# Performance work log

Hardware: AMD Instinct MI355X
Metric: run time of the kernel (lower is better)

## Reference

```python
import jax, jax.numpy as jnp
import numpy as np

B, L, C_IN = 32, 244, 128
F_NUM, KS = 64, 5
HID = 512
SA_DIV = 3
F3 = F_NUM * 3
D_SA = F3 // SA_DIV  # must equal F_NUM (sa_div==3) for the view in SelfAttention


def setup_inputs() -> dict:
    key = jax.random.key(0)
    ks = jax.random.split(key, 16)

    def rn(k, shape, fan_in):
        return jax.random.normal(k, shape, dtype=jnp.float32) * float(np.sqrt(2.0 / fan_in))

    return {
        "x": jax.random.normal(ks[0], (B, L, C_IN), dtype=jnp.float32),
        "conv1_w": rn(ks[1], (F_NUM, 1, KS, 1), KS),
        "conv1_b": jnp.zeros((F_NUM,), jnp.float32),
        "conv2_w": rn(ks[2], (F_NUM, F_NUM, KS, 1), F_NUM * KS),
        "conv2_b": jnp.zeros((F_NUM,), jnp.float32),
        "conv3_w": rn(ks[3], (F_NUM, F_NUM, KS, 1), F_NUM * KS),
        "conv3_b": jnp.zeros((F_NUM,), jnp.float32),
        "conv4_w": rn(ks[4], (F_NUM, F_NUM, KS, 1), F_NUM * KS),
        "conv4_b": jnp.zeros((F_NUM,), jnp.float32),
        "wq": rn(ks[5], (D_SA, F3), F3),
        "wk": rn(ks[6], (D_SA, F3), F3),
        "wv": rn(ks[7], (D_SA, F3), F3),
        "wv1": rn(ks[8], (D_SA, F3), F3),
        "gamma": jnp.full((1,), 0.1, jnp.float32),
        "gru_wih": rn(ks[9], (3 * HID, F_NUM * C_IN), F_NUM * C_IN),
        "gru_whh": rn(ks[10], (3 * HID, HID), HID),
        "gru_bih": jnp.zeros((3 * HID,), jnp.float32),
        "gru_bhh": jnp.zeros((3 * HID,), jnp.float32),
        "fc_w": rn(ks[11], (1, HID), HID),
        "fc_b": jnp.zeros((1,), jnp.float32),
    }


def _conv2d(x, w, b):
    y = jax.lax.conv_general_dilated(
        x, w, window_strides=(1, 1), padding="VALID",
        dimension_numbers=("NCHW", "OIHW", "NCHW"))
    return y + b[None, :, None, None]


def reference(x, conv1_w, conv1_b, conv2_w, conv2_b, conv3_w, conv3_b, conv4_w, conv4_b,
              wq, wk, wv, wv1, gamma, gru_wih, gru_whh, gru_bih, gru_bhh, fc_w, fc_b):
    # conv stack: (B,1,L,C) -> (B,F,L',C), time dim shrinks by 4*(KS-1)
    h = x[:, None, :, :]
    h = jax.nn.relu(_conv2d(h, conv1_w, conv1_b))
    h = jax.nn.relu(_conv2d(h, conv2_w, conv2_b))
    h = jax.nn.relu(_conv2d(h, conv3_w, conv3_b))
    h = jax.nn.relu(_conv2d(h, conv4_w, conv4_b))
    Bn, Fn, Lp, Cn = h.shape
    step = int(np.ceil(Lp / 3))
    # static slice starts; last slice is x[:, :, -3:, :] (matches torch loop)
    starts = np.minimum(np.arange(step) * 3, Lp - 3)
    idx = starts[:, None] + np.arange(3)                               # (S,3)
    xs = h[:, :, idx, :]                                               # (B,F,S,3,C)
    xs = xs.transpose(0, 2, 1, 3, 4).reshape(Bn, step, Fn * 3, Cn)     # (B,S,F3,C)
    # batched SelfAttention (1x1 conv1d == matmul over channel dim)
    f = jnp.einsum("df,bsfc->bsdc", wq, xs)
    g = jnp.einsum("df,bsfc->bsdc", wk, xs)
    v = jnp.einsum("df,bsfc->bsdc", wv, xs)
    v1 = jnp.einsum("df,bsfc->bsdc", wv1, xs)
    # torch: softmax(bmm(f^T, g), dim=1) -> softmax over first C axis
    beta = jax.nn.softmax(jnp.einsum("bsdc,bsdk->bsck", f, g), axis=-2)
    o = gamma[0] * jnp.einsum("bsdc,bsck->bsdk", v, beta) + v1         # (B,S,F,C)
    seq = o.transpose(1, 0, 2, 3).reshape(step, Bn, Fn * Cn)           # (S,B,F*C)
    # single-layer GRU (PyTorch gate order r,z,n), seq-first
    xg = jnp.einsum("sbi,gi->sbg", seq, gru_wih) + gru_bih             # (S,B,3H)

    def gru_step(hprev, xg_t):
        hg = hprev @ gru_whh.T + gru_bhh
        xr, xz, xn = jnp.split(xg_t, 3, axis=-1)
        hr, hz, hn = jnp.split(hg, 3, axis=-1)
        r = jax.nn.sigmoid(xr + hr)
        z = jax.nn.sigmoid(xz + hz)
        n = jnp.tanh(xn + r * hn)
        hnew = (1.0 - z) * n + z * hprev
        return hnew, hnew

    h0 = jnp.zeros((Bn, HID), seq.dtype)
    _, outs = jax.lax.scan(gru_step, h0, xg)                            # (S,B,H)
    # temporal attention pooling over the time axis (axis 0)
    att = jnp.einsum("sbh,h->sb", outs, fc_w[0]) + fc_b[0]
    w_att = jax.nn.softmax(att, axis=0)[:, :, None]
    return jnp.sum(w_att * outs, axis=0)                                # (B,H)
```

## Files before the change

kernel.cpp:

```cpp
#include <hip/hip_runtime.h>
#include <math.h>


typedef __attribute__((ext_vector_type(8))) short short8;
typedef __attribute__((ext_vector_type(4))) float f32x4;

#define XG_STRIDE 3735552ull

__device__ inline float sigm(float x){ return 1.f/(1.f+__expf(-x)); }
__device__ inline unsigned short f2bf(float f){
    unsigned int u = __float_as_uint(f);
    u = (u + 0x7FFFu + ((u >> 16) & 1u)) >> 16;
    return (unsigned short)u;
}
__device__ inline float bf2f(unsigned short h){
    return __uint_as_float(((unsigned int)h) << 16);
}

__global__ __launch_bounds__(256) void conv1_k(const float* __restrict__ x,
        unsigned short* __restrict__ out_h, unsigned short* __restrict__ out_l,
        const float* __restrict__ w1, const float* __restrict__ b1, int b_base)
{
    __shared__ float w1s[320];
    __shared__ float b1s[64];
    int t = threadIdx.x;
    for (int idx = t; idx < 320; idx += 256) w1s[idx] = w1[idx];
    if (t < 64)  b1s[t] = b1[t];
    __syncthreads();
    int i = blockIdx.x*256 + t;
    int c = i & 127; int t2 = i >> 7;
    int l = t2 % 240; int b = t2 / 240;
    const float* xp = x + ((size_t)(b_base + b)*244 + l)*128 + c;
    float xv[5];
    #pragma unroll
    for (int k=0;k<5;++k) xv[k] = xp[k*128];
    unsigned short* oh = out_h + (size_t)i*64;
    unsigned short* ol = out_l + (size_t)i*64;
    #pragma unroll
    for (int f8=0; f8<8; ++f8){
        unsigned short rh[8], rl[8];
        #pragma unroll
        for (int j=0;j<8;++j){
            int f = f8*8 + j;
            float a = b1s[f];
            #pragma unroll
            for (int k=0;k<5;++k) a += w1s[f*5+k]*xv[k];
            a = a > 0.f ? a : 0.f;
            unsigned short hi = f2bf(a);
            rh[j] = hi;
            rl[j] = f2bf(a - bf2f(hi));
        }
        *(short8*)(oh + f8*8) = *(short8*)rh;
        *(short8*)(ol + f8*8) = *(short8*)rl;
    }
}

__global__ __launch_bounds__(256) void repack_convw_k(const float* __restrict__ w2,
        const float* __restrict__ w3, const float* __restrict__ w4,
        unsigned short* __restrict__ wbf_h, unsigned short* __restrict__ wbf_l)
{
    int idx = blockIdx.x*256 + threadIdx.x;
    int fi = idx & 63; int t2 = idx >> 6;
    int fo = t2 & 63;  int t3 = t2 >> 6;
    int k = t3 % 5;    int layer = t3 / 5;
    const float* ws_ = (layer==0)? w2 : (layer==1)? w3 : w4;
    float v = ws_[(fo*64 + fi)*5 + k];
    unsigned short hi = f2bf(v);
    wbf_h[idx] = hi;
    wbf_l[idx] = f2bf(v - bf2f(hi));
}

__global__ __launch_bounds__(256) void conv_mfma_s(
        const unsigned short* __restrict__ in_h, const unsigned short* __restrict__ in_l,
        unsigned short* __restrict__ out_h, unsigned short* __restrict__ out_l,
        const unsigned short* __restrict__ wk_h, const unsigned short* __restrict__ wk_l,
        const float* __restrict__ bias, int Lin, int Lout)
{
    __shared__ __align__(16) unsigned short Abh[128*72], Abl[128*72];
    __shared__ __align__(16) unsigned short Wbh[64*72],  Wbl[64*72];
    int t = threadIdx.x;
    int l = blockIdx.x, b = blockIdx.y;
    int lane = t & 63, w = t >> 6;
    int lr = lane & 15, lh = lane >> 4;
    f32x4 acc[2][4];
    #pragma unroll
    for (int mf=0;mf<2;++mf)
        #pragma unroll
        for (int nf=0;nf<4;++nf) acc[mf][nf] = (f32x4)0.f;

    const size_t ib = ((size_t)b*Lin + l)*8192;
    for (int k=0;k<5;++k){
        __syncthreads();
        #pragma unroll
        for (int i=0;i<4;++i){
            int idx = i*256 + t; int row = idx>>3, c8 = idx&7;
            *(short8*)&Abh[row*72 + c8*8] = *(const short8*)(in_h + ib + (size_t)k*8192 + idx*8);
            *(short8*)&Abl[row*72 + c8*8] = *(const short8*)(in_l + ib + (size_t)k*8192 + idx*8);
        }
        #pragma unroll
        for (int i=0;i<2;++i){
            int idx = i*256 + t; int row = idx>>3, c8 = idx&7;
            *(short8*)&Wbh[row*72 + c8*8] = *(const short8*)(wk_h + k*4096 + idx*8);
            *(short8*)&Wbl[row*72 + c8*8] = *(const short8*)(wk_l + k*4096 + idx*8);
        }
        __syncthreads();
        #pragma unroll
        for (int kk=0;kk<2;++kk){
            short8 ah[2], al[2], bh[4], blo[4];
            #pragma unroll
            for (int mf=0;mf<2;++mf){
                ah[mf] = *(const short8*)&Abh[(w*32+mf*16+lr)*72 + kk*32 + lh*8];
                al[mf] = *(const short8*)&Abl[(w*32+mf*16+lr)*72 + kk*32 + lh*8];
            }
            #pragma unroll
            for (int nf=0;nf<4;++nf){
                bh[nf]  = *(const short8*)&Wbh[(nf*16+lr)*72 + kk*32 + lh*8];
                blo[nf] = *(const short8*)&Wbl[(nf*16+lr)*72 + kk*32 + lh*8];
            }
            #pragma unroll
            for (int mf=0;mf<2;++mf)
                #pragma unroll
                for (int nf=0;nf<4;++nf){
                    acc[mf][nf] = __builtin_amdgcn_mfma_f32_16x16x32_bf16(ah[mf], bh[nf],  acc[mf][nf], 0,0,0);
                    acc[mf][nf] = __builtin_amdgcn_mfma_f32_16x16x32_bf16(ah[mf], blo[nf], acc[mf][nf], 0,0,0);
                    acc[mf][nf] = __builtin_amdgcn_mfma_f32_16x16x32_bf16(al[mf], bh[nf],  acc[mf][nf], 0,0,0);
                }
        }
    }
    const size_t ob = ((size_t)b*Lout + l)*8192;
    #pragma unroll
    for (int nf=0;nf<4;++nf){
        int fo = nf*16 + lr;
        float bv = bias[fo];
        #pragma unroll
        for (int mf=0;mf<2;++mf)
            #pragma unroll
            for (int q=0;q<4;++q){
                int c = w*32 + mf*16 + lh*4 + q;
                float v = acc[mf][nf][q] + bv;
                v = v > 0.f ? v : 0.f;
                unsigned short hi = f2bf(v);
                out_h[ob + c*64 + fo] = hi;
                out_l[ob + c*64 + fo] = f2bf(v - bf2f(hi));
            }
    }
}

__global__ __launch_bounds__(256) void repack_wrep_k(const float* __restrict__ wq,
        const float* __restrict__ wk, const float* __restrict__ wv,
        const float* __restrict__ wv1,
        unsigned short* __restrict__ wr_h, unsigned short* __restrict__ wr_l)
{
    int idx = blockIdx.x*256 + threadIdx.x;
    int ko = idx % 192; int md = idx / 192;
    int m = md >> 6, d = md & 63;
    int jj = ko >> 6, f = ko & 63;
    const float* src = (m==0)? wq : (m==1)? wk : (m==2)? wv : wv1;
    float v = src[d*192 + f*3 + jj];
    unsigned short hi = f2bf(v);
    wr_h[idx] = hi;
    wr_l[idx] = f2bf(v - bf2f(hi));
}

__global__ __launch_bounds__(256) void project_mfma_s(
        const unsigned short* __restrict__ h_h, const unsigned short* __restrict__ h_l,
        const unsigned short* __restrict__ wr_h, const unsigned short* __restrict__ wr_l,
        float* __restrict__ Fo, float* __restrict__ Go,
        float* __restrict__ Vo, float* __restrict__ V1o)
{
    __shared__ __align__(16) unsigned short Abh[128*72], Abl[128*72];
    __shared__ __align__(16) unsigned short Bbh[64*72],  Bbl[64*72];
    int t = threadIdx.x;
    int s = blockIdx.x, bl = blockIdx.y, mz = blockIdx.z;
    int lane = t & 63, w = t >> 6;
    int wm = w >> 1, wn = w & 1;
    int lr = lane & 15, lh = lane >> 4;
    f32x4 acc[4][2];
    #pragma unroll
    for (int mf=0;mf<4;++mf)
        #pragma unroll
        for (int nf=0;nf<2;++nf) acc[mf][nf] = (f32x4)0.f;

    for (int jj=0;jj<3;++jj){
        __syncthreads();
        const size_t ao_ = ((size_t)bl*228 + 3*s + jj)*8192;
        #pragma unroll
        for (int i=0;i<4;++i){
            int idx = i*256 + t; int row = idx>>3, c8 = idx&7;
            *(short8*)&Abh[row*72 + c8*8] = *(const short8*)(h_h + ao_ + idx*8);
            *(short8*)&Abl[row*72 + c8*8] = *(const short8*)(h_l + ao_ + idx*8);
        }
        #pragma unroll
        for (int i=0;i<2;++i){
            int idx = i*256 + t; int row = idx>>3, c8 = idx&7;
            size_t wo = (size_t)(mz*64 + row)*192 + jj*64 + c8*8;
            *(short8*)&Bbh[row*72 + c8*8] = *(const short8*)(wr_h + wo);
            *(short8*)&Bbl[row*72 + c8*8] = *(const short8*)(wr_l + wo);
        }
        __syncthreads();
        #pragma unroll
        for (int kk=0;kk<2;++kk){
            short8 ah[4], al[4], bh[2], blo[2];
            #pragma unroll
            for (int mf=0;mf<4;++mf){
                ah[mf] = *(const short8*)&Abh[(wm*64+mf*16+lr)*72 + kk*32 + lh*8];
                al[mf] = *(const short8*)&Abl[(wm*64+mf*16+lr)*72 + kk*32 + lh*8];
            }
            #pragma unroll
            for (int nf=0;nf<2;++nf){
                bh[nf]  = *(const short8*)&Bbh[(wn*32+nf*16+lr)*72 + kk*32 + lh*8];
                blo[nf] = *(const short8*)&Bbl[(wn*32+nf*16+lr)*72 + kk*32 + lh*8];
            }
            #pragma unroll
            for (int mf=0;mf<4;++mf)
                #pragma unroll
                for (int nf=0;nf<2;++nf){
                    acc[mf][nf] = __builtin_amdgcn_mfma_f32_16x16x32_bf16(ah[mf], bh[nf],  acc[mf][nf], 0,0,0);
                    acc[mf][nf] = __builtin_amdgcn_mfma_f32_16x16x32_bf16(ah[mf], blo[nf], acc[mf][nf], 0,0,0);
                    acc[mf][nf] = __builtin_amdgcn_mfma_f32_16x16x32_bf16(al[mf], bh[nf],  acc[mf][nf], 0,0,0);
                }
        }
    }
    float* dst = (mz==0)? Fo : (mz==1)? Go : (mz==2)? Vo : V1o;
    size_t bs = (size_t)bl*76 + s;
    #pragma unroll
    for (int mf=0;mf<4;++mf)
        #pragma unroll
        for (int nf=0;nf<2;++nf){
            int d = wn*32 + nf*16 + lr;
            int c0 = wm*64 + mf*16 + lh*4;
            *(f32x4*)&dst[(bs*64 + d)*128 + c0] = acc[mf][nf];
        }
}

__global__ __launch_bounds__(256) void attend_k(const float* __restrict__ Fg,
        const float* __restrict__ Gg, const float* __restrict__ Vg,
        const float* __restrict__ V1g, const float* __restrict__ gamma,
        unsigned short* __restrict__ seq_bf, int b_base)
{
    __shared__ float sm[16384];
    int t = threadIdx.x;
    int s = blockIdx.x, bl = blockIdx.y;
    size_t base = ((size_t)bl*76 + s)*8192;
    for (int i=t; i<8192; i+=256) sm[i]      = Fg[base+i];
    for (int i=t; i<8192; i+=256) sm[8192+i] = Gg[base+i];
    __syncthreads();

    int k = t & 127, ch = t >> 7;
    float sc[64];
    #pragma unroll
    for (int j=0;j<64;++j) sc[j]=0.f;
    for (int d=0; d<64; ++d){
        float gk = sm[8192 + d*128 + k];
        #pragma unroll
        for (int cj=0; cj<16; ++cj){
            float4 f4 = *(const float4*)&sm[d*128 + ch*64 + cj*4];
            sc[cj*4+0] += f4.x*gk; sc[cj*4+1] += f4.y*gk;
            sc[cj*4+2] += f4.z*gk; sc[cj*4+3] += f4.w*gk;
        }
    }
    __syncthreads();
    float m = -1e30f;
    #pragma unroll
    for (int j=0;j<64;++j) m = fmaxf(m, sc[j]);
    sm[t] = m;
    for (int i=t; i<8192; i+=256) sm[8192+i] = Vg[base+i];
    __syncthreads();
    m = fmaxf(sm[k], sm[128+k]);
    float lsum = 0.f;
    #pragma unroll
    for (int j=0;j<64;++j){ sc[j] = __expf(sc[j]-m); lsum += sc[j]; }
    __syncthreads();
    sm[t] = lsum;
    __syncthreads();
    float rinv = 1.f/(sm[k] + sm[128+k]);
    #pragma unroll
    for (int j=0;j<64;++j) sc[j] *= rinv;
    __syncthreads();

    if (ch == 0){
        #pragma unroll
        for (int j=0;j<64;++j) sm[j*128 + k] = sc[j];
    }
    __syncthreads();

    int k2 = t & 31, dq = t >> 5;
    float ao[8][4];
    #pragma unroll
    for (int j=0;j<8;++j)
        #pragma unroll
        for (int mm=0;mm<4;++mm) ao[j][mm]=0.f;

    for (int c2=0; c2<64; ++c2){
        float bv0 = sm[c2*128 + k2],    bv1 = sm[c2*128 + k2+32];
        float bv2 = sm[c2*128 + k2+64], bv3 = sm[c2*128 + k2+96];
        #pragma unroll
        for (int j=0;j<8;++j){
            float v = sm[8192 + (dq*8+j)*128 + c2];
            ao[j][0]+=v*bv0; ao[j][1]+=v*bv1; ao[j][2]+=v*bv2; ao[j][3]+=v*bv3;
        }
    }
    __syncthreads();
    if (ch == 1){
        #pragma unroll
        for (int j=0;j<64;++j) sm[j*128 + k] = sc[j];
    }
    __syncthreads();
    for (int c2=64; c2<128; ++c2){
        float bv0 = sm[(c2-64)*128 + k2],    bv1 = sm[(c2-64)*128 + k2+32];
        float bv2 = sm[(c2-64)*128 + k2+64], bv3 = sm[(c2-64)*128 + k2+96];
        #pragma unroll
        for (int j=0;j<8;++j){
            float v = sm[8192 + (dq*8+j)*128 + c2];
            ao[j][0]+=v*bv0; ao[j][1]+=v*bv1; ao[j][2]+=v*bv2; ao[j][3]+=v*bv3;
        }
    }

    float gm = gamma[0];
    size_t sbase = (size_t)(s*32 + b_base + bl)*8192;
    #pragma unroll
    for (int j=0;j<8;++j){
        int d = dq*8+j;
        #pragma unroll
        for (int mm=0;mm<4;++mm){
            int kk = k2 + 32*mm;
            float val = gm*ao[j][mm] + V1g[base + (size_t)d*128 + kk];
            seq_bf[sbase + (size_t)d*128 + kk] = f2bf(val);
        }
    }
}

__global__ __launch_bounds__(256) void conv_wih_bf16(const float* __restrict__ w,
        unsigned short* __restrict__ o)
{
    int i = (blockIdx.x*256 + threadIdx.x)*4;
    float4 v = *(const float4*)&w[i];
    ushort4 r;
    r.x = f2bf(v.x); r.y = f2bf(v.y); r.z = f2bf(v.z); r.w = f2bf(v.w);
    *(ushort4*)&o[i] = r;
}

__global__ __launch_bounds__(512) void gemm_xg_mfma(const unsigned short* __restrict__ A,
        const unsigned short* __restrict__ Bw, const float* __restrict__ bih,
        float* __restrict__ out, int nsplit)
{
    __shared__ float AsF[128*36];
    __shared__ float BsF[128*36];
    int nwg = 228*nsplit;
    int orig = blockIdx.x;
    int q = nwg >> 3, rr8 = nwg & 7;
    int xcd = orig & 7, i8 = orig >> 3;
    int wgid = (xcd < rr8 ? xcd*(q+1) : rr8*(q+1) + (xcd-rr8)*q) + i8;
    int kz = wgid / 228;
    int r2 = wgid % 228;
    int n0 = (r2 % 12) * 128, m0 = (r2 / 12) * 128;
    int klen = 8192 / nsplit;
    int kbase = kz * klen;
    int nkt = klen >> 6;

    int t = threadIdx.x;
    int w = t >> 6;
    int wm = w >> 1, wn = w & 1;
    int lane = t & 63, lr = lane & 15, lh = lane >> 4;

    f32x4 acc[2][4];
    #pragma unroll
    for (int mi=0;mi<2;++mi)
        #pragma unroll
        for (int ni=0;ni<4;++ni) acc[mi][ni] = (f32x4)0.f;

    float4 ra[2], rb[2];
    #pragma unroll
    for (int i=0;i<2;++i){
        int idx = i*512 + t; int row = idx>>3, seg = idx&7;
        ra[i] = *(const float4*)(A  + (size_t)(m0 + row)*8192 + kbase + seg*8);
        rb[i] = *(const float4*)(Bw + (size_t)(n0 + row)*8192 + kbase + seg*8);
    }
    for (int kt=0; kt<nkt; ++kt){
        __syncthreads();
        #pragma unroll
        for (int i=0;i<2;++i){
            int idx = i*512 + t; int row = idx>>3, seg = idx&7;
            *(float4*)&AsF[row*36 + seg*4] = ra[i];
            *(float4*)&BsF[row*36 + seg*4] = rb[i];
        }
        __syncthreads();
        if (kt < nkt-1){
            int k0 = kbase + (kt+1)*64;
            #pragma unroll
            for (int i=0;i<2;++i){
                int idx = i*512 + t; int row = idx>>3, seg = idx&7;
                ra[i] = *(const float4*)(A  + (size_t)(m0 + row)*8192 + k0 + seg*8);
                rb[i] = *(const float4*)(Bw + (size_t)(n0 + row)*8192 + k0 + seg*8);
            }
        }
        #pragma unroll
        for (int kk=0;kk<2;++kk){
            short8 af[2], bf_[4];
            #pragma unroll
            for (int mi=0;mi<2;++mi)
                af[mi] = *(short8*)&AsF[(wm*32 + mi*16 + lr)*36 + kk*16 + lh*4];
            #pragma unroll
            for (int ni=0;ni<4;++ni)
                bf_[ni] = *(short8*)&BsF[(wn*64 + ni*16 + lr)*36 + kk*16 + lh*4];
            #pragma unroll
            for (int mi=0;mi<2;++mi)
                #pragma unroll
                for (int ni=0;ni<4;++ni)
                    acc[mi][ni] = __builtin_amdgcn_mfma_f32_16x16x32_bf16(
                                      af[mi], bf_[ni], acc[mi][ni], 0, 0, 0);
        }
    }
    float* op = out + (size_t)kz*XG_STRIDE;
    #pragma unroll
    for (int ni=0;ni<4;++ni){
        int n = n0 + wn*64 + ni*16 + lr;
        float bv = (kz == 0) ? bih[n] : 0.f;
        #pragma unroll
        for (int mi=0;mi<2;++mi){
            #pragma unroll
            for (int q2=0;q2<4;++q2){
                int m = m0 + wm*32 + mi*16 + lh*4 + q2;
                op[(size_t)m*1536 + n] = acc[mi][ni][q2] + bv;
            }
        }
    }
}

__global__ __launch_bounds__(256) void build_whhp_k(const float* __restrict__ whh,
        float4* __restrict__ whh_p)
{
    int idx = blockIdx.x*256 + threadIdx.x;
    int i = idx >> 9, j = idx & 511;
    float4 o;
    o.x = whh[(size_t)j*512 + i];
    o.y = whh[(size_t)(512+j)*512 + i];
    o.z = whh[(size_t)(1024+j)*512 + i];
    o.w = 0.f;
    whh_p[idx] = o;
}

__global__ __launch_bounds__(1024) void gru_step_k(const float4* __restrict__ whh_p,
        const float* __restrict__ xg, const float* __restrict__ bhh,
        float* __restrict__ outs, int s, int nsplit)
{
    __shared__ float hl[2048];
    __shared__ float red[4][4][64][3];
    int t = threadIdx.x;
    int jc = blockIdx.x & 7, bq = blockIdx.x >> 3;
    for (int idx=t; idx<2048; idx+=1024)
        hl[idx] = outs[(size_t)s*16384 + (size_t)(bq*4 + (idx>>9))*512 + (idx&511)];
    __syncthreads();
    int jl = t & 63, bl = (t >> 6) & 3, iq = t >> 8;
    int j = jc*64 + jl;
    float a0=0.f,a1=0.f,a2=0.f;
    const float4* wp = whh_p + (size_t)(iq*128)*512 + j;
    const float* hb = hl + bl*512 + iq*128;
    #pragma unroll 4
    for (int i=0;i<128;++i){
        float4 w4 = wp[(size_t)i*512];
        float hv = hb[i];
        a0 += w4.x*hv; a1 += w4.y*hv; a2 += w4.z*hv;
    }
    red[iq][bl][jl][0] = a0; red[iq][bl][jl][1] = a1; red[iq][bl][jl][2] = a2;
    __syncthreads();
    if (t < 256){
        int jl2 = t & 63, bl2 = t >> 6;
        int j2 = jc*64 + jl2, b = bq*4 + bl2;
        float hr=0.f, hz=0.f, hn=0.f;
        #pragma unroll
        for (int q=0;q<4;++q){
            hr += red[q][bl2][jl2][0];
            hz += red[q][bl2][jl2][1];
            hn += red[q][bl2][jl2][2];
        }
        size_t xi = (size_t)(s*32 + b)*1536 + j2;
        float xr = xg[xi], xz = xg[xi+512], xn = xg[xi+1024];
        if (nsplit == 2){
            xr += xg[xi + XG_STRIDE];
            xz += xg[xi + 512 + XG_STRIDE];
            xn += xg[xi + 1024 + XG_STRIDE];
        }
        hr += bhh[j2]; hz += bhh[512+j2]; hn += bhh[1024+j2];
        float r = sigm(xr+hr), z = sigm(xz+hz);
        float n = tanhf(xn + r*hn);
        float hp = hl[bl2*512 + j2];
        float hnew = (1.f - z)*n + z*hp;
        outs[(size_t)(s+1)*16384 + (size_t)b*512 + j2] = hnew;
    }
}

__global__ __launch_bounds__(256) void pool_k(const float* __restrict__ outs,
        const float* __restrict__ fcw, const float* __restrict__ fcb,
        float* __restrict__ out)
{
    __shared__ float att[80], watt[128];
    int b = blockIdx.x, t = threadIdx.x;
    int w = t >> 6, lane = t & 63;
    for (int s = w; s < 76; s += 4){
        float acc = 0.f;
        const float* op = outs + (size_t)(s+1)*16384 + (size_t)b*512;
        #pragma unroll
        for (int hh = 0; hh < 512; hh += 64) acc += op[hh+lane]*fcw[hh+lane];
        #pragma unroll
        for (int off=32; off; off>>=1) acc += __shfl_down(acc, off);
        if (lane==0) att[s] = acc + fcb[0];
    }
    __syncthreads();
    if (t < 64){
        float a0 = (t<76)? att[t] : -1e30f;
        float a1 = (t+64<76)? att[t+64] : -1e30f;
        float m = fmaxf(a0,a1);
        #pragma unroll
        for (int off=32; off; off>>=1) m = fmaxf(m, __shfl_xor(m, off));
        float e0 = (t<76)? __expf(a0-m) : 0.f;
        float e1 = (t+64<76)? __expf(a1-m) : 0.f;
        float ssum = e0+e1;
        #pragma unroll
        for (int off=32; off; off>>=1) ssum += __shfl_xor(ssum, off);
        float ri = 1.f/ssum;
        watt[t] = e0*ri;
        watt[t+64] = e1*ri;
    }
    __syncthreads();
    for (int h = t; h < 512; h += 256){
        float acc=0.f;
        for (int s=0;s<76;++s) acc += watt[s]*outs[(size_t)(s+1)*16384 + (size_t)b*512 + h];
        out[(size_t)b*512 + h] = acc;
    }
}

extern "C" void kernel_launch(void* const* d_in, const int* in_sizes, int n_in,
                              void* d_out, int out_size, void* d_ws, size_t ws_size,
                              hipStream_t stream)
{
    const float* x   = (const float*)d_in[0];
    const float* w1  = (const float*)d_in[1];  const float* b1  = (const float*)d_in[2];
    const float* w2  = (const float*)d_in[3];  const float* b2  = (const float*)d_in[4];
    const float* w3  = (const float*)d_in[5];  const float* b3  = (const float*)d_in[6];
    const float* w4  = (const float*)d_in[7];  const float* b4  = (const float*)d_in[8];
    const float* wq  = (const float*)d_in[9];  const float* wk  = (const float*)d_in[10];
    const float* wv  = (const float*)d_in[11]; const float* wv1 = (const float*)d_in[12];
    const float* gamma = (const float*)d_in[13];
    const float* wih = (const float*)d_in[14]; const float* whh = (const float*)d_in[15];
    const float* bih = (const float*)d_in[16]; const float* bhh = (const float*)d_in[17];
    const float* fcw = (const float*)d_in[18]; const float* fcb = (const float*)d_in[19];

    int nb = 2, ns = 1;
    if      (ws_size >= (8ull*4521984ull + 16117760ull + 3735552ull)*4ull + 4096){ nb = 8; ns = 2; }
    else if (ws_size >= (4ull*4521984ull + 16117760ull + 3735552ull)*4ull + 4096){ nb = 4; ns = 2; }
    else if (ws_size >= (2ull*4521984ull + 16117760ull + 3735552ull)*4ull + 4096){ nb = 2; ns = 2; }

    float* ws = (float*)d_ws;
    size_t off = 0;
    size_t szAh = (size_t)nb*983040ull;
    size_t szBh = (size_t)nb*966656ull;
    size_t szP  = (size_t)nb*622592ull;
    unsigned short* bufAh = (unsigned short*)(ws + off); off += szAh;
    unsigned short* bufAl = (unsigned short*)(ws + off); off += szAh;
    unsigned short* bufBh = (unsigned short*)(ws + off); off += szBh;
    unsigned short* bufBl = (unsigned short*)(ws + off); off += szBh;
    float* V1b = ws + off; off += szP;
    unsigned short* seq_bf = (unsigned short*)(ws + off); off += 9961472ull;
    float* xg   = ws + off; off += (size_t)ns*XG_STRIDE;
    float* outs = ws + off; off += 77ull*16384;
    float4* whh_p = (float4*)(ws + off); off += 1048576ull;
    unsigned short* wbf_h = (unsigned short*)(ws + off); off += 30720ull;
    unsigned short* wbf_l = (unsigned short*)(ws + off); off += 30720ull;
    unsigned short* wr_h  = (unsigned short*)(ws + off); off += 24576ull;
    unsigned short* wr_l  = (unsigned short*)(ws + off); off += 24576ull;

    float* Fb = (float*)bufAh;
    float* Gb = Fb + szP;
    float* Vb = Fb + 2*szP;
    unsigned short* wih_bf = bufAh;

    repack_convw_k<<<240, 256, 0, stream>>>(w2, w3, w4, wbf_h, wbf_l);
    repack_wrep_k<<<192, 256, 0, stream>>>(wq, wk, wv, wv1, wr_h, wr_l);
    build_whhp_k<<<1024, 256, 0, stream>>>(whh, whh_p);
    hipMemsetAsync(outs, 0, 16384*sizeof(float), stream);

    int nchunks = 32 / nb;
    for (int chunk=0; chunk<nchunks; ++chunk){
        int b_base = chunk*nb;
        conv1_k<<<nb*120, 256, 0, stream>>>(x, bufAh, bufAl, w1, b1, b_base);
        conv_mfma_s<<<dim3(236,nb), 256, 0, stream>>>(bufAh, bufAl, bufBh, bufBl,
                                                      wbf_h, wbf_l, b2, 240, 236);
        conv_mfma_s<<<dim3(232,nb), 256, 0, stream>>>(bufBh, bufBl, bufAh, bufAl,
                                                      wbf_h+20480, wbf_l+20480, b3, 236, 232);
        conv_mfma_s<<<dim3(228,nb), 256, 0, stream>>>(bufAh, bufAl, bufBh, bufBl,
                                                      wbf_h+40960, wbf_l+40960, b4, 232, 228);
        project_mfma_s<<<dim3(76,nb,4), 256, 0, stream>>>(bufBh, bufBl, wr_h, wr_l,
                                                          Fb, Gb, Vb, V1b);
        attend_k<<<dim3(76,nb), 256, 0, stream>>>(Fb, Gb, Vb, V1b, gamma, seq_bf, b_base);
    }
    conv_wih_bf16<<<12288, 256, 0, stream>>>(wih, wih_bf);
    gemm_xg_mfma<<<228*ns, 512, 0, stream>>>(seq_bf, wih_bf, bih, xg, ns);
    for (int s=0; s<76; ++s)
        gru_step_k<<<64, 1024, 0, stream>>>(whh_p, xg, bhh, outs, s, ns);
    pool_k<<<32, 256, 0, stream>>>(outs, fcw, fcb, (float*)d_out);
}
```

Before: 2.999 ms.

## Split conv and projection tiles over channel halves; vectorize xg GEMM stores

The conv and projection MFMA kernels now split the 128-column C dimension across two blocks using a new grid z dimension. This halves each block's tile and LDS footprint, doubles the block count and raises occupancy. In exchange, the weight tile is loaded twice as often. The xg GEMM swaps its MFMA operands so that each lane holds four consecutive N outputs, which lets the bias add and the stores use float4 instead of scalar strided writes.

```diff
diff --git a/kernel.cpp b/kernel.cpp
--- a/kernel.cpp
+++ b/kernel.cpp
@@ -76,23 +76,21 @@
         const unsigned short* __restrict__ wk_h, const unsigned short* __restrict__ wk_l,
         const float* __restrict__ bias, int Lin, int Lout)
 {
-    __shared__ __align__(16) unsigned short Abh[128*72], Abl[128*72];
-    __shared__ __align__(16) unsigned short Wbh[64*72],  Wbl[64*72];
+    __shared__ __align__(16) unsigned short Abh[64*72], Abl[64*72];
+    __shared__ __align__(16) unsigned short Wbh[64*72], Wbl[64*72];
     int t = threadIdx.x;
-    int l = blockIdx.x, b = blockIdx.y;
+    int l = blockIdx.x, b = blockIdx.y, ch = blockIdx.z;
     int lane = t & 63, w = t >> 6;
     int lr = lane & 15, lh = lane >> 4;
-    f32x4 acc[2][4];
-    #pragma unroll
-    for (int mf=0;mf<2;++mf)
-        #pragma unroll
-        for (int nf=0;nf<4;++nf) acc[mf][nf] = (f32x4)0.f;
-
-    const size_t ib = ((size_t)b*Lin + l)*8192;
+    f32x4 acc[4];
+    #pragma unroll
+    for (int nf=0;nf<4;++nf) acc[nf] = (f32x4)0.f;
+
+    const size_t ib = ((size_t)b*Lin + l)*8192 + (size_t)ch*4096;
     for (int k=0;k<5;++k){
         __syncthreads();
         #pragma unroll
-        for (int i=0;i<4;++i){
+        for (int i=0;i<2;++i){
             int idx = i*256 + t; int row = idx>>3, c8 = idx&7;
             *(short8*)&Abh[row*72 + c8*8] = *(const short8*)(in_h + ib + (size_t)k*8192 + idx*8);
             *(short8*)&Abl[row*72 + c8*8] = *(const short8*)(in_l + ib + (size_t)k*8192 + idx*8);
@@ -106,25 +104,20 @@
         __syncthreads();
         #pragma unroll
         for (int kk=0;kk<2;++kk){
-            short8 ah[2], al[2], bh[4], blo[4];
-            #pragma unroll
-            for (int mf=0;mf<2;++mf){
-                ah[mf] = *(const short8*)&Abh[(w*32+mf*16+lr)*72 + kk*32 + lh*8];
-                al[mf] = *(const short8*)&Abl[(w*32+mf*16+lr)*72 + kk*32 + lh*8];
-            }
+            short8 ah, al, bh[4], blo[4];
+            ah = *(const short8*)&Abh[(w*16+lr)*72 + kk*32 + lh*8];
+            al = *(const short8*)&Abl[(w*16+lr)*72 + kk*32 + lh*8];
             #pragma unroll
             for (int nf=0;nf<4;++nf){
                 bh[nf]  = *(const short8*)&Wbh[(nf*16+lr)*72 + kk*32 + lh*8];
                 blo[nf] = *(const short8*)&Wbl[(nf*16+lr)*72 + kk*32 + lh*8];
             }
             #pragma unroll
-            for (int mf=0;mf<2;++mf)
-                #pragma unroll
-                for (int nf=0;nf<4;++nf){
-                    acc[mf][nf] = __builtin_amdgcn_mfma_f32_16x16x32_bf16(ah[mf], bh[nf],  acc[mf][nf], 0,0,0);
-                    acc[mf][nf] = __builtin_amdgcn_mfma_f32_16x16x32_bf16(ah[mf], blo[nf], acc[mf][nf], 0,0,0);
-                    acc[mf][nf] = __builtin_amdgcn_mfma_f32_16x16x32_bf16(al[mf], bh[nf],  acc[mf][nf], 0,0,0);
-                }
+            for (int nf=0;nf<4;++nf){
+                acc[nf] = __builtin_amdgcn_mfma_f32_16x16x32_bf16(ah, bh[nf],  acc[nf], 0,0,0);
+                acc[nf] = __builtin_amdgcn_mfma_f32_16x16x32_bf16(ah, blo[nf], acc[nf], 0,0,0);
+                acc[nf] = __builtin_amdgcn_mfma_f32_16x16x32_bf16(al, bh[nf],  acc[nf], 0,0,0);
+            }
         }
     }
     const size_t ob = ((size_t)b*Lout + l)*8192;
@@ -133,16 +126,14 @@
         int fo = nf*16 + lr;
         float bv = bias[fo];
         #pragma unroll
-        for (int mf=0;mf<2;++mf)
-            #pragma unroll
-            for (int q=0;q<4;++q){
-                int c = w*32 + mf*16 + lh*4 + q;
-                float v = acc[mf][nf][q] + bv;
-                v = v > 0.f ? v : 0.f;
-                unsigned short hi = f2bf(v);
-                out_h[ob + c*64 + fo] = hi;
-                out_l[ob + c*64 + fo] = f2bf(v - bf2f(hi));
-            }
+        for (int q=0;q<4;++q){
+            int c = ch*64 + w*16 + lh*4 + q;
+            float v = acc[nf][q] + bv;
+            v = v > 0.f ? v : 0.f;
+            unsigned short hi = f2bf(v);
+            out_h[ob + c*64 + fo] = hi;
+            out_l[ob + c*64 + fo] = f2bf(v - bf2f(hi));
+        }
     }
 }
 
@@ -168,24 +159,25 @@
         float* __restrict__ Fo, float* __restrict__ Go,
         float* __restrict__ Vo, float* __restrict__ V1o)
 {
-    __shared__ __align__(16) unsigned short Abh[128*72], Abl[128*72];
-    __shared__ __align__(16) unsigned short Bbh[64*72],  Bbl[64*72];
+    __shared__ __align__(16) unsigned short Abh[64*72], Abl[64*72];
+    __shared__ __align__(16) unsigned short Bbh[64*72], Bbl[64*72];
     int t = threadIdx.x;
-    int s = blockIdx.x, bl = blockIdx.y, mz = blockIdx.z;
+    int s = blockIdx.x, bl = blockIdx.y;
+    int mz = blockIdx.z >> 1, mh = blockIdx.z & 1;
     int lane = t & 63, w = t >> 6;
     int wm = w >> 1, wn = w & 1;
     int lr = lane & 15, lh = lane >> 4;
-    f32x4 acc[4][2];
-    #pragma unroll
-    for (int mf=0;mf<4;++mf)
+    f32x4 acc[2][2];
+    #pragma unroll
+    for (int mf=0;mf<2;++mf)
         #pragma unroll
         for (int nf=0;nf<2;++nf) acc[mf][nf] = (f32x4)0.f;
 
     for (int jj=0;jj<3;++jj){
         __syncthreads();
-        const size_t ao_ = ((size_t)bl*228 + 3*s + jj)*8192;
-        #pragma unroll
-        for (int i=0;i<4;++i){
+        const size_t ao_ = ((size_t)bl*228 + 3*s + jj)*8192 + (size_t)mh*4096;
+        #pragma unroll
+        for (int i=0;i<2;++i){
             int idx = i*256 + t; int row = idx>>3, c8 = idx&7;
             *(short8*)&Abh[row*72 + c8*8] = *(const short8*)(h_h + ao_ + idx*8);
             *(short8*)&Abl[row*72 + c8*8] = *(const short8*)(h_l + ao_ + idx*8);
@@ -200,11 +192,11 @@
         __syncthreads();
         #pragma unroll
         for (int kk=0;kk<2;++kk){
-            short8 ah[4], al[4], bh[2], blo[2];
-            #pragma unroll
-            for (int mf=0;mf<4;++mf){
-                ah[mf] = *(const short8*)&Abh[(wm*64+mf*16+lr)*72 + kk*32 + lh*8];
-                al[mf] = *(const short8*)&Abl[(wm*64+mf*16+lr)*72 + kk*32 + lh*8];
+            short8 ah[2], al[2], bh[2], blo[2];
+            #pragma unroll
+            for (int mf=0;mf<2;++mf){
+                ah[mf] = *(const short8*)&Abh[(wm*32+mf*16+lr)*72 + kk*32 + lh*8];
+                al[mf] = *(const short8*)&Abl[(wm*32+mf*16+lr)*72 + kk*32 + lh*8];
             }
             #pragma unroll
             for (int nf=0;nf<2;++nf){
@@ -212,7 +204,7 @@
                 blo[nf] = *(const short8*)&Bbl[(wn*32+nf*16+lr)*72 + kk*32 + lh*8];
             }
             #pragma unroll
-            for (int mf=0;mf<4;++mf)
+            for (int mf=0;mf<2;++mf)
                 #pragma unroll
                 for (int nf=0;nf<2;++nf){
                     acc[mf][nf] = __builtin_amdgcn_mfma_f32_16x16x32_bf16(ah[mf], bh[nf],  acc[mf][nf], 0,0,0);
@@ -224,11 +216,11 @@
     float* dst = (mz==0)? Fo : (mz==1)? Go : (mz==2)? Vo : V1o;
     size_t bs = (size_t)bl*76 + s;
     #pragma unroll
-    for (int mf=0;mf<4;++mf)
+    for (int mf=0;mf<2;++mf)
         #pragma unroll
         for (int nf=0;nf<2;++nf){
             int d = wn*32 + nf*16 + lr;
-            int c0 = wm*64 + mf*16 + lh*4;
+            int c0 = mh*64 + wm*32 + mf*16 + lh*4;
             *(f32x4*)&dst[(bs*64 + d)*128 + c0] = acc[mf][nf];
         }
 }
@@ -408,21 +400,24 @@
                 #pragma unroll
                 for (int ni=0;ni<4;++ni)
                     acc[mi][ni] = __builtin_amdgcn_mfma_f32_16x16x32_bf16(
-                                      af[mi], bf_[ni], acc[mi][ni], 0, 0, 0);
+                                      bf_[ni], af[mi], acc[mi][ni], 0, 0, 0);
         }
     }
     float* op = out + (size_t)kz*XG_STRIDE;
     #pragma unroll
     for (int ni=0;ni<4;++ni){
-        int n = n0 + wn*64 + ni*16 + lr;
-        float bv = (kz == 0) ? bih[n] : 0.f;
+        int nbase = n0 + wn*64 + ni*16 + lh*4;
+        float4 bi4 = (kz == 0) ? *(const float4*)&bih[nbase]
+                               : make_float4(0.f,0.f,0.f,0.f);
         #pragma unroll
         for (int mi=0;mi<2;++mi){
-            #pragma unroll
-            for (int q2=0;q2<4;++q2){
-                int m = m0 + wm*32 + mi*16 + lh*4 + q2;
-                op[(size_t)m*1536 + n] = acc[mi][ni][q2] + bv;
-            }
+            int m = m0 + wm*32 + mi*16 + lr;
+            float4 o;
+            o.x = acc[mi][ni][0] + bi4.x;
+            o.y = acc[mi][ni][1] + bi4.y;
+            o.z = acc[mi][ni][2] + bi4.z;
+            o.w = acc[mi][ni][3] + bi4.w;
+            *(float4*)&op[(size_t)m*1536 + nbase] = o;
         }
     }
 }
@@ -584,13 +579,13 @@
     for (int chunk=0; chunk<nchunks; ++chunk){
         int b_base = chunk*nb;
         conv1_k<<<nb*120, 256, 0, stream>>>(x, bufAh, bufAl, w1, b1, b_base);
-        conv_mfma_s<<<dim3(236,nb), 256, 0, stream>>>(bufAh, bufAl, bufBh, bufBl,
-                                                      wbf_h, wbf_l, b2, 240, 236);
-        conv_mfma_s<<<dim3(232,nb), 256, 0, stream>>>(bufBh, bufBl, bufAh, bufAl,
-                                                      wbf_h+20480, wbf_l+20480, b3, 236, 232);
-        conv_mfma_s<<<dim3(228,nb), 256, 0, stream>>>(bufAh, bufAl, bufBh, bufBl,
-                                                      wbf_h+40960, wbf_l+40960, b4, 232, 228);
-        project_mfma_s<<<dim3(76,nb,4), 256, 0, stream>>>(bufBh, bufBl, wr_h, wr_l,
+        conv_mfma_s<<<dim3(236,nb,2), 256, 0, stream>>>(bufAh, bufAl, bufBh, bufBl,
+                                                        wbf_h, wbf_l, b2, 240, 236);
+        conv_mfma_s<<<dim3(232,nb,2), 256, 0, stream>>>(bufBh, bufBl, bufAh, bufAl,
+                                                        wbf_h+20480, wbf_l+20480, b3, 236, 232);
+        conv_mfma_s<<<dim3(228,nb,2), 256, 0, stream>>>(bufAh, bufAl, bufBh, bufBl,
+                                                        wbf_h+40960, wbf_l+40960, b4, 232, 228);
+        project_mfma_s<<<dim3(76,nb,8), 256, 0, stream>>>(bufBh, bufBl, wr_h, wr_l,
                                                           Fb, Gb, Vb, V1b);
         attend_k<<<dim3(76,nb), 256, 0, stream>>>(Fb, Gb, Vb, V1b, gamma, seq_bf, b_base);
     }
```

Result: no change. 2.998 ms (-0.0%).
